# Performance work log

Measured on AMD Instinct MI355X. Metric: run time of the kernel, lower is better.

The kernel has to match this reference:

```python
import jax, jax.numpy as jnp
import numpy as np

B, L, D_MODEL = 2, 1024, 1024
EXPAND = 2
D_INNER = EXPAND * D_MODEL      # 2048
D_STATE = 16
D_CONV = 4
DT_RANK = D_MODEL // 16         # 64


def setup_inputs() -> dict:
    key = jax.random.key(0)
    ks = jax.random.split(key, 8)
    s = 0.02
    x = jax.random.normal(ks[0], (B, L, D_MODEL), jnp.float32)
    W_in = (jax.random.normal(ks[1], (D_MODEL, 2 * D_INNER), jnp.float32) * s)
    conv_w = jax.random.normal(ks[2], (D_INNER, 1, D_CONV), jnp.float32) * 0.2  # depthwise kernel (O,I/g,K)
    conv_b = jnp.zeros((D_INNER,), jnp.float32)
    W_xproj = jax.random.normal(ks[3], (D_INNER, DT_RANK + 2 * D_STATE), jnp.float32) * s
    W_dt = jax.random.normal(ks[4], (DT_RANK, D_INNER), jnp.float32) * (DT_RANK ** -0.5)
    b_dt = jnp.full((D_INNER,), -4.6, jnp.float32)  # softplus^{-1}(~0.01), mamba-style dt init
    A_log = jnp.log(jnp.broadcast_to(jnp.arange(1, D_STATE + 1, dtype=jnp.float32), (D_INNER, D_STATE)))
    D_skip = jnp.ones((D_INNER,), jnp.float32)
    W_out = jax.random.normal(ks[5], (D_INNER, D_MODEL), jnp.float32) * s
    return dict(x=x, W_in=W_in, conv_w=conv_w, conv_b=conv_b, W_xproj=W_xproj,
                W_dt=W_dt, b_dt=b_dt, A_log=A_log, D_skip=D_skip, W_out=W_out)


def _mamba(x, W_in, conv_w, conv_b, W_xproj, W_dt, b_dt, A_log, D_skip, W_out):
    b, l, _ = x.shape
    # input projection and gate split
    xz = jnp.einsum('bld,de->ble', x, W_in)            # (B, L, 2*d_inner)
    x_in, z = jnp.split(xz, 2, axis=-1)                # each (B, L, d_inner)
    # causal depthwise conv1d + SiLU
    xt = jnp.transpose(x_in, (0, 2, 1))                # (B, d_inner, L)
    xt = jnp.pad(xt, ((0, 0), (0, 0), (D_CONV - 1, 0)))
    conv = jax.lax.conv_general_dilated(
        xt, conv_w, window_strides=(1,), padding='VALID',
        dimension_numbers=('NCH', 'OIH', 'NCH'), feature_group_count=D_INNER)
    conv = conv + conv_b[None, :, None]                # (B, d_inner, L)
    u = jax.nn.silu(jnp.transpose(conv, (0, 2, 1)))    # (B, L, d_inner)
    # input-dependent SSM parameters
    x_dbl = jnp.einsum('bld,de->ble', u, W_xproj)      # (B, L, dt_rank + 2*d_state)
    dt_lr = x_dbl[..., :DT_RANK]
    Bm = x_dbl[..., DT_RANK:DT_RANK + D_STATE]         # (B, L, d_state)
    Cm = x_dbl[..., DT_RANK + D_STATE:]                # (B, L, d_state)
    delta = jax.nn.softplus(jnp.einsum('blr,rd->bld', dt_lr, W_dt) + b_dt)  # (B, L, d_inner)
    A = -jnp.exp(A_log)                                # (d_inner, d_state)
    dA = jnp.exp(jnp.einsum('bld,dn->bldn', delta, A))           # (B, L, d_inner, d_state)
    dBu = (delta * u)[..., None] * Bm[:, :, None, :]              # (B, L, d_inner, d_state)
    # selective scan over time
    def step(h, inp):
        dA_t, dBu_t, C_t = inp
        h = dA_t * h + dBu_t                           # (B, d_inner, d_state)
        y_t = jnp.einsum('bdn,bn->bd', h, C_t)
        return h, y_t
    h0 = jnp.zeros((b, D_INNER, D_STATE), x.dtype)
    _, ys = jax.lax.scan(step, h0, (jnp.swapaxes(dA, 0, 1), jnp.swapaxes(dBu, 0, 1), jnp.swapaxes(Cm, 0, 1)))
    y = jnp.swapaxes(ys, 0, 1)                          # (B, L, d_inner)
    y = y + D_skip * u
    y = y * jax.nn.silu(z)
    out = jnp.einsum('bld,de->ble', y, W_out)           # (B, L, d_model)
    return out  # dropout is identity in eval mode


def reference(x, W_in, conv_w, conv_b, W_xproj, W_dt, b_dt, A_log, D_skip, W_out):
    return _mamba(x, W_in, conv_w, conv_b, W_xproj, W_dt, b_dt, A_log, D_skip, W_out)
```

## Files before the change

### kernel.cpp

```cpp
#include <hip/hip_runtime.h>
#include <cmath>

#define B_  2
#define L_  1024
#define DM  1024
#define DI  2048
#define DS  16
#define DR  64
#define NC  32
#define CL  (L_/NC)

typedef __attribute__((ext_vector_type(8))) short short8;
typedef __attribute__((ext_vector_type(4))) float f32x4;

static __device__ __forceinline__ ushort f2bf(float f) {
    union { float f; unsigned u; } c; c.f = f;
    unsigned u = c.u;
    return (ushort)((u + 0x7fffu + ((u >> 16) & 1u)) >> 16);
}
static __device__ __forceinline__ float bf2f(ushort h) {
    union { unsigned u; float f; } c; c.u = ((unsigned)h) << 16;
    return c.f;
}

static __device__ __forceinline__ float softplus_f(float v) {
    return (v > 20.f) ? v : log1pf(__expf(v));
}

static __device__ void bt_body(const float* __restrict__ in,
                               ushort* __restrict__ oh, ushort* __restrict__ ol,
                               int K, int N, int Npad, int bx, int by,
                               float (*t)[33])
{
    const int tid = threadIdx.x;
    const int tx = tid & 31, ty = tid >> 5;
    const int n0 = bx * 32, k0 = by * 32;
    #pragma unroll
    for (int i = 0; i < 4; ++i) {
        int k = k0 + ty * 4 + i, n = n0 + tx;
        t[ty * 4 + i][tx] = (n < N) ? in[(size_t)k * N + n] : 0.f;
    }
    __syncthreads();
    #pragma unroll
    for (int i = 0; i < 4; ++i) {
        int r = n0 + ty * 4 + i;
        int c = k0 + tx;
        if (r < Npad) {
            float v = t[tx][ty * 4 + i];
            ushort h = f2bf(v);
            oh[(size_t)r * K + c] = h;
            if (ol) ol[(size_t)r * K + c] = f2bf(v - bf2f(h));
        }
    }
}

__global__ __launch_bounds__(256) void prep_all(
    const float* __restrict__ x, const float* __restrict__ W_in,
    const float* __restrict__ W_xprj, const float* __restrict__ W_dt,
    ushort* __restrict__ Xh, ushort* __restrict__ WIh, ushort* __restrict__ WIl,
    ushort* __restrict__ WXh, ushort* __restrict__ WXl,
    ushort* __restrict__ WDh, ushort* __restrict__ WDl)
{
    __shared__ float t[32][33];
    int blk = blockIdx.x;
    if (blk < 4096) {
        bt_body(W_in, WIh, WIl, 1024, 4096, 4096, blk & 127, blk >> 7, t);
    } else if (blk < 4352) {
        int b2 = blk - 4096;
        bt_body(W_xprj, WXh, WXl, 2048, 96, 128, b2 & 3, b2 >> 2, t);
    } else if (blk < 4480) {
        int b2 = blk - 4352;
        bt_body(W_dt, WDh, WDl, 64, 2048, 2048, b2 & 63, b2 >> 6, t);
    } else {
        int v = (blk - 4480) * 256 + threadIdx.x;
        int r  = v >> 7;
        int c8 = v & 127;
        const float* p = x + (size_t)r * DM + c8 * 8;
        float4 v0 = *(const float4*)p;
        float4 v1 = *(const float4*)(p + 4);
        float vv[8] = {v0.x, v0.y, v0.z, v0.w, v1.x, v1.y, v1.z, v1.w};
        unsigned h[4];
        #pragma unroll
        for (int j = 0; j < 4; ++j)
            h[j] = (unsigned)f2bf(vv[2*j]) | ((unsigned)f2bf(vv[2*j+1]) << 16);
        size_t o = (size_t)r * 1024 + c8 * 8;
        *(uint4*)&Xh[o] = make_uint4(h[0], h[1], h[2], h[3]);
    }
}

__global__ __launch_bounds__(256) void convBT(
    const float* __restrict__ in, ushort* __restrict__ oh,
    int K, int N, int Npad)
{
    __shared__ float t[32][33];
    bt_body(in, oh, nullptr, K, N, Npad, blockIdx.x, blockIdx.y, t);
}

static __device__ __forceinline__ void stage_tile(
    ushort* lds, const ushort* __restrict__ g, int ld, int row0, int k0,
    int wid, int lane)
{
    #pragma unroll
    for (int it = 0; it < 2; ++it) {
        int o  = wid * 2048 + it * 1024;
        int ob = o + lane * 16;
        int a  = ob ^ (((ob >> 7) & 7) << 4);
        int row = a >> 6;
        int lc  = (a >> 4) & 3;
        const ushort* gp = g + (size_t)(row0 + row) * ld + k0 + lc * 8;
        __builtin_amdgcn_global_load_lds(
            (const __attribute__((address_space(1))) void*)gp,
            (__attribute__((address_space(3))) void*)((char*)lds + o),
            16, 0, 0);
    }
}

template<int TERMS>
static __device__ __forceinline__ void stage_all(
    ushort* buf, const ushort* Ah, const ushort* Bh, const ushort* Bl,
    int lda, int ldb, int bm, int bn, int k, int wid, int lane)
{
    stage_tile(buf,        Ah, lda, bm, k, wid, lane);
    stage_tile(buf + 4096, Bh, ldb, bn, k, wid, lane);
    if (TERMS == 2) stage_tile(buf + 8192, Bl, ldb, bn, k, wid, lane);
}

static __device__ __forceinline__ short8 frag(const ushort* lds, int row, int fq) {
    int a = row * 64 + fq * 16;
    int b = a ^ (((a >> 7) & 7) << 4);
    return *(const short8*)((const char*)lds + b);
}

template<int TERMS>
static __device__ __forceinline__ void compute_tile(
    const ushort* buf, int wr, int wc, int fr, int fq, f32x4 acc[4][4])
{
    const ushort* sAh = buf;
    const ushort* sBh = buf + 4096;
    const ushort* sBl = buf + 8192;
    short8 a_h[4], b_h[4], b_l[4];
    #pragma unroll
    for (int m = 0; m < 4; ++m)
        a_h[m] = frag(sAh, wr + m * 16 + fr, fq);
    #pragma unroll
    for (int n = 0; n < 4; ++n) {
        b_h[n] = frag(sBh, wc + n * 16 + fr, fq);
        if (TERMS == 2) b_l[n] = frag(sBl, wc + n * 16 + fr, fq);
    }
    #pragma unroll
    for (int m = 0; m < 4; ++m)
        #pragma unroll
        for (int n = 0; n < 4; ++n) {
            acc[m][n] = __builtin_amdgcn_mfma_f32_16x16x32_bf16(a_h[m], b_h[n], acc[m][n], 0, 0, 0);
            if (TERMS == 2)
                acc[m][n] = __builtin_amdgcn_mfma_f32_16x16x32_bf16(a_h[m], b_l[n], acc[m][n], 0, 0, 0);
        }
}

template<int TERMS, int EPI>
__global__ __launch_bounds__(256) void gemm_bt(
    const ushort* __restrict__ Ah,
    const ushort* __restrict__ Bh, const ushort* __restrict__ Bl,
    float* __restrict__ C, ushort* __restrict__ oh, ushort* __restrict__ ol,
    const float* __restrict__ bvec,
    int M, int N, int lda, int ldb, int ldc, int kspl)
{
    constexpr int TILE = TERMS == 1 ? 8192 : 12288;
    __shared__ ushort sm[2 * TILE];

    const int tid = threadIdx.x, wid = tid >> 6, lane = tid & 63;
    const int bm = blockIdx.y * 128, bn = blockIdx.x * 128;
    const int kb = blockIdx.z * kspl;
    const int wr = (wid >> 1) * 64, wc = (wid & 1) * 64;
    const int fr = lane & 15, fq = lane >> 4;

    f32x4 acc[4][4] = {};

    stage_all<TERMS>(sm, Ah, Bh, Bl, lda, ldb, bm, bn, kb, wid, lane);
    __syncthreads();
    int cur = 0;
    for (int k0 = 32; k0 < kspl; k0 += 32) {
        ushort* nbuf       = cur ? sm : sm + TILE;
        const ushort* cbuf = cur ? sm + TILE : sm;
        stage_all<TERMS>(nbuf, Ah, Bh, Bl, lda, ldb, bm, bn, kb + k0, wid, lane);
        compute_tile<TERMS>(cbuf, wr, wc, fr, fq, acc);
        __syncthreads();
        cur ^= 1;
    }
    compute_tile<TERMS>(cur ? sm + TILE : sm, wr, wc, fr, fq, acc);

    #pragma unroll
    for (int m = 0; m < 4; ++m) {
        int rbase = bm + wr + m * 16 + fq * 4;
        #pragma unroll
        for (int n = 0; n < 4; ++n) {
            int col = bn + wc + n * 16 + fr;
            if (col >= N) continue;
            if (EPI == 0) {
                #pragma unroll
                for (int j = 0; j < 4; ++j)
                    C[((size_t)blockIdx.z * M + rbase + j) * ldc + col] = acc[m][n][j];
            } else {
                float bb = bvec[col];
                #pragma unroll
                for (int j = 0; j < 4; ++j) {
                    float v = softplus_f(acc[m][n][j] + bb);
                    ushort hh = f2bf(v);
                    size_t off = (size_t)(rbase + j) * ldc + col;
                    oh[off] = hh;
                    ol[off] = f2bf(v - bf2f(hh));
                }
            }
        }
    }
}

__global__ __launch_bounds__(256) void reduce_xproj(
    const float* __restrict__ p, float* __restrict__ xdbl,
    ushort* __restrict__ DTh)
{
    int i = blockIdx.x * 256 + threadIdx.x;
    if (i >= 2048 * 96) return;
    float s = 0.f;
    #pragma unroll
    for (int c = 0; c < 8; ++c) s += p[i + (size_t)c * (2048 * 96)];
    xdbl[i] = s;
    int row = i / 96, col = i - row * 96;
    if (col < 64) DTh[row * 64 + col] = f2bf(s);
}

__global__ __launch_bounds__(256) void reduceN(
    const float* __restrict__ p, float* __restrict__ o, int n, int nch)
{
    int i = blockIdx.x * 256 + threadIdx.x;
    if (i >= n) return;
    float s = 0.f;
    for (int c = 0; c < nch; ++c) s += p[i + (size_t)c * n];
    o[i] = s;
}

__global__ __launch_bounds__(256) void conv_silu(
    const float* __restrict__ xz, const float* __restrict__ w,
    const float* __restrict__ bias, ushort* __restrict__ uh,
    ushort* __restrict__ ul)
{
    int idx = blockIdx.x * 256 + threadIdx.x;
    if (idx >= B_ * L_ * DI) return;
    int d  = idx & (DI - 1);
    int bl = idx >> 11;
    int l  = bl & (L_ - 1);

    const float w0 = w[d * 4 + 0], w1 = w[d * 4 + 1];
    const float w2 = w[d * 4 + 2], w3 = w[d * 4 + 3];
    float s = bias[d];
    size_t base = (size_t)bl * 4096 + d;
    if (l >= 3) s = fmaf(w0, xz[base - 3 * 4096], s);
    if (l >= 2) s = fmaf(w1, xz[base - 2 * 4096], s);
    if (l >= 1) s = fmaf(w2, xz[base - 1 * 4096], s);
    s = fmaf(w3, xz[base], s);
    float v = s / (1.f + __expf(-s));
    ushort h = f2bf(v);
    uh[idx] = h;
    ul[idx] = f2bf(v - bf2f(h));
}

__global__ __launch_bounds__(256) void scan_partial(
    const ushort* __restrict__ Dh, const ushort* __restrict__ Dl,
    const ushort* __restrict__ uh, const ushort* __restrict__ ul,
    const float* __restrict__ xdbl, const float* __restrict__ A_log,
    float* __restrict__ sA, float* __restrict__ sH)
{
    __shared__ float Bs[CL][16];
    const int tid  = threadIdx.x;
    const int dblk = blockIdx.x & 7;
    const int c    = (blockIdx.x >> 3) & (NC - 1);
    const int b    = blockIdx.x >> 8;
    const int d    = dblk * 256 + tid;
    const int bl0  = b * L_ + c * CL;

    for (int i = tid; i < CL * 16; i += 256) {
        int t = i >> 4, n = i & 15;
        Bs[t][n] = xdbl[(size_t)(bl0 + t) * 96 + DR + n];
    }
    __syncthreads();

    float Adn[16];
    #pragma unroll
    for (int q = 0; q < 4; ++q) {
        float4 al = *(const float4*)&A_log[d * DS + q * 4];
        Adn[q * 4 + 0] = -__expf(al.x);
        Adn[q * 4 + 1] = -__expf(al.y);
        Adn[q * 4 + 2] = -__expf(al.z);
        Adn[q * 4 + 3] = -__expf(al.w);
    }
    float h[16];
    #pragma unroll
    for (int n = 0; n < 16; ++n) h[n] = 0.f;
    float S = 0.f;

    size_t pd = (size_t)bl0 * DI + d;
    for (int t = 0; t < CL; ++t) {
        float dv = bf2f(Dh[pd]) + bf2f(Dl[pd]);
        float uv = bf2f(uh[pd]) + bf2f(ul[pd]);
        float du = dv * uv;
        S += dv;
        float Bv[16];
        *(float4*)&Bv[0]  = *(const float4*)&Bs[t][0];
        *(float4*)&Bv[4]  = *(const float4*)&Bs[t][4];
        *(float4*)&Bv[8]  = *(const float4*)&Bs[t][8];
        *(float4*)&Bv[12] = *(const float4*)&Bs[t][12];
        #pragma unroll
        for (int n = 0; n < 16; ++n) {
            float dA = __expf(dv * Adn[n]);
            h[n] = fmaf(dA, h[n], du * Bv[n]);
        }
        pd += DI;
    }

    size_t o = (((size_t)c * B_ + b) * DI + d) * DS;
    float aP[16], hh[16];
    #pragma unroll
    for (int n = 0; n < 16; ++n) { aP[n] = __expf(S * Adn[n]); hh[n] = h[n]; }
    #pragma unroll
    for (int q = 0; q < 4; ++q) {
        *(float4*)&sA[o + q * 4] = *(float4*)&aP[q * 4];
        *(float4*)&sH[o + q * 4] = *(float4*)&hh[q * 4];
    }
}

__global__ __launch_bounds__(256) void scan_combine(
    const float* __restrict__ sA, const float* __restrict__ sH,
    float* __restrict__ hinit)
{
    int idx = blockIdx.x * 256 + threadIdx.x;
    int n = idx & 15;
    int d = (idx >> 4) & (DI - 1);
    int b = idx >> 15;
    float h = 0.f;
    #pragma unroll
    for (int c = 0; c < NC; ++c) {
        size_t o = (((size_t)c * B_ + b) * DI + d) * DS + n;
        hinit[o] = h;
        h = fmaf(sA[o], h, sH[o]);
    }
}

__global__ __launch_bounds__(256) void scan_final(
    const ushort* __restrict__ Dh, const ushort* __restrict__ Dl,
    const ushort* __restrict__ uh, const ushort* __restrict__ ul,
    const float* __restrict__ xdbl, const float* __restrict__ xz,
    const float* __restrict__ A_log, const float* __restrict__ D_skip,
    const float* __restrict__ hinit, ushort* __restrict__ yh)
{
    __shared__ float Bs[CL][16];
    __shared__ float Cs[CL][16];
    const int tid  = threadIdx.x;
    const int dblk = blockIdx.x & 7;
    const int c    = (blockIdx.x >> 3) & (NC - 1);
    const int b    = blockIdx.x >> 8;
    const int d    = dblk * 256 + tid;
    const int bl0  = b * L_ + c * CL;

    for (int i = tid; i < CL * 16; i += 256) {
        int t = i >> 4, n = i & 15;
        size_t px = (size_t)(bl0 + t) * 96 + DR + n;
        Bs[t][n] = xdbl[px];
        Cs[t][n] = xdbl[px + DS];
    }
    __syncthreads();

    float Adn[16];
    #pragma unroll
    for (int q = 0; q < 4; ++q) {
        float4 al = *(const float4*)&A_log[d * DS + q * 4];
        Adn[q * 4 + 0] = -__expf(al.x);
        Adn[q * 4 + 1] = -__expf(al.y);
        Adn[q * 4 + 2] = -__expf(al.z);
        Adn[q * 4 + 3] = -__expf(al.w);
    }
    const float Dd = D_skip[d];

    float h[16];
    size_t o = (((size_t)c * B_ + b) * DI + d) * DS;
    #pragma unroll
    for (int q = 0; q < 4; ++q)
        *(float4*)&h[q * 4] = *(const float4*)&hinit[o + q * 4];

    size_t pd = (size_t)bl0 * DI + d;
    size_t pz = (size_t)bl0 * 4096 + 2048 + d;
    for (int t = 0; t < CL; ++t) {
        float dv = bf2f(Dh[pd]) + bf2f(Dl[pd]);
        float uv = bf2f(uh[pd]) + bf2f(ul[pd]);
        float du = dv * uv;
        float Bv[16], Cv[16];
        *(float4*)&Bv[0]  = *(const float4*)&Bs[t][0];
        *(float4*)&Bv[4]  = *(const float4*)&Bs[t][4];
        *(float4*)&Bv[8]  = *(const float4*)&Bs[t][8];
        *(float4*)&Bv[12] = *(const float4*)&Bs[t][12];
        *(float4*)&Cv[0]  = *(const float4*)&Cs[t][0];
        *(float4*)&Cv[4]  = *(const float4*)&Cs[t][4];
        *(float4*)&Cv[8]  = *(const float4*)&Cs[t][8];
        *(float4*)&Cv[12] = *(const float4*)&Cs[t][12];
        float acc = 0.f;
        #pragma unroll
        for (int n = 0; n < 16; ++n) {
            float dA = __expf(dv * Adn[n]);
            h[n] = fmaf(dA, h[n], du * Bv[n]);
            acc = fmaf(h[n], Cv[n], acc);
        }
        float zv = xz[pz];
        float yv = acc + Dd * uv;
        yv *= zv / (1.f + __expf(-zv));
        yh[pd] = f2bf(yv);
        pd += DI; pz += 4096;
    }
}

extern "C" void kernel_launch(void* const* d_in, const int* in_sizes, int n_in,
                              void* d_out, int out_size, void* d_ws, size_t ws_size,
                              hipStream_t stream)
{
    const float* x      = (const float*)d_in[0];
    const float* W_in   = (const float*)d_in[1];
    const float* conv_w = (const float*)d_in[2];
    const float* conv_b = (const float*)d_in[3];
    const float* W_xprj = (const float*)d_in[4];
    const float* W_dt   = (const float*)d_in[5];
    const float* b_dt   = (const float*)d_in[6];
    const float* A_log  = (const float*)d_in[7];
    const float* D_skip = (const float*)d_in[8];
    const float* W_out  = (const float*)d_in[9];
    float* out = (float*)d_out;

    char* ws = (char*)d_ws;
    float*  xz    = (float*)(ws + 0);
    ushort* Dh    = (ushort*)(ws + 33554432);
    ushort* Dl    = (ushort*)(ws + 41943040);
    float*  xdbl  = (float*)(ws + 50331648);
    ushort* Xh    = (ushort*)(ws + 57409536);
    float*  parts = (float*)(ws + 57409536);
    ushort* WIh   = (ushort*)(ws + 65798144);
    ushort* WIl   = (ushort*)(ws + 74186752);
    float*  sA    = (float*)(ws + 57409536);
    float*  sH    = (float*)(ws + 65798144);
    float*  hin   = (float*)(ws + 74186752);
    ushort* Yh    = (ushort*)(ws + 57409536);
    float*  parts2= (float*)(ws + 65798144);
    ushort* Uh    = (ushort*)(ws + 82575360);
    ushort* Ul    = (ushort*)(ws + 90963968);
    ushort* Woh   = (ushort*)(ws + 82575360);
    ushort* WXh   = (ushort*)(ws + 99352576);
    ushort* WXl   = (ushort*)(ws + 99876864);
    ushort* DTh   = (ushort*)(ws + 100401152);
    ushort* WDh   = (ushort*)(ws + 100914176);
    ushort* WDl   = (ushort*)(ws + 101170688);

    dim3 blk(256);
    const int M = B_ * L_;

    prep_all<<<dim3(5504), blk, 0, stream>>>(
        x, W_in, W_xprj, W_dt, Xh, WIh, WIl, WXh, WXl, WDh, WDl);

    gemm_bt<2, 0><<<dim3(32, 16, 1), blk, 0, stream>>>(
        Xh, WIh, WIl, xz, nullptr, nullptr, nullptr,
        M, 4096, DM, DM, 4096, DM);

    conv_silu<<<dim3((B_ * L_ * DI) / 256), blk, 0, stream>>>(xz, conv_w, conv_b, Uh, Ul);

    gemm_bt<2, 0><<<dim3(1, 16, 8), blk, 0, stream>>>(
        Uh, WXh, WXl, parts, nullptr, nullptr, nullptr,
        M, 96, DI, DI, 96, 256);
    reduce_xproj<<<dim3(768), blk, 0, stream>>>(parts, xdbl, DTh);

    gemm_bt<2, 1><<<dim3(16, 16, 1), blk, 0, stream>>>(
        DTh, WDh, WDl, nullptr, Dh, Dl, b_dt,
        M, DI, DR, DR, DI, DR);

    scan_partial<<<dim3(B_ * NC * 8), blk, 0, stream>>>(
        Dh, Dl, Uh, Ul, xdbl, A_log, sA, sH);
    scan_combine<<<dim3((B_ * DI * DS) / 256), blk, 0, stream>>>(sA, sH, hin);
    scan_final<<<dim3(B_ * NC * 8), blk, 0, stream>>>(
        Dh, Dl, Uh, Ul, xdbl, xz, A_log, D_skip, hin, Yh);

    convBT<<<dim3(DM / 32, DI / 32), blk, 0, stream>>>(W_out, Woh, DI, DM, DM);
    gemm_bt<1, 0><<<dim3(8, 16, 2), blk, 0, stream>>>(
        Yh, Woh, nullptr, parts2, nullptr, nullptr, nullptr,
        M, DM, DI, DI, DM, 1024);
    reduceN<<<dim3(2097152 / 256), blk, 0, stream>>>(parts2, out, M * DM, 2);
}
```

Measured before the change: 204.5 us.

## Drop W_in low-bf16 term and replace split-K out GEMM with 128x64 tile kernel

The input projection GEMM now uses only the high bf16 part of W_in, which removes the hi/lo error-compensation term and the WIl conversion writes. This halves the B-operand staging and MFMA work for the largest GEMM, at the cost of lower precision in xz. The output projection changes from a split-K=2 GEMM followed by a reduction kernel to a dedicated 128x64-tile double-buffered kernel that writes the output directly. That drops the partial buffer traffic and one launch, and raises the block count to 256 so the work still spreads across the GPU.

```diff
diff --git a/kernel.cpp b/kernel.cpp
--- a/kernel.cpp
+++ b/kernel.cpp
@@ -57,14 +57,14 @@
 __global__ __launch_bounds__(256) void prep_all(
     const float* __restrict__ x, const float* __restrict__ W_in,
     const float* __restrict__ W_xprj, const float* __restrict__ W_dt,
-    ushort* __restrict__ Xh, ushort* __restrict__ WIh, ushort* __restrict__ WIl,
+    ushort* __restrict__ Xh, ushort* __restrict__ WIh,
     ushort* __restrict__ WXh, ushort* __restrict__ WXl,
     ushort* __restrict__ WDh, ushort* __restrict__ WDl)
 {
     __shared__ float t[32][33];
     int blk = blockIdx.x;
     if (blk < 4096) {
-        bt_body(W_in, WIh, WIl, 1024, 4096, 4096, blk & 127, blk >> 7, t);
+        bt_body(W_in, WIh, nullptr, 1024, 4096, 4096, blk & 127, blk >> 7, t);
     } else if (blk < 4352) {
         int b2 = blk - 4096;
         bt_body(W_xprj, WXh, WXl, 2048, 96, 128, b2 & 3, b2 >> 2, t);
@@ -115,6 +115,28 @@
     }
 }
 
+static __device__ __forceinline__ void stage_tile64(
+    ushort* lds, const ushort* __restrict__ g, int ld, int row0, int k0,
+    int wid, int lane)
+{
+    int o  = wid * 1024;
+    int ob = o + lane * 16;
+    int a  = ob ^ (((ob >> 7) & 7) << 4);
+    int row = a >> 6;
+    int lc  = (a >> 4) & 3;
+    const ushort* gp = g + (size_t)(row0 + row) * ld + k0 + lc * 8;
+    __builtin_amdgcn_global_load_lds(
+        (const __attribute__((address_space(1))) void*)gp,
+        (__attribute__((address_space(3))) void*)((char*)lds + o),
+        16, 0, 0);
+}
+
+static __device__ __forceinline__ short8 frag(const ushort* lds, int row, int fq) {
+    int a = row * 64 + fq * 16;
+    int b = a ^ (((a >> 7) & 7) << 4);
+    return *(const short8*)((const char*)lds + b);
+}
+
 template<int TERMS>
 static __device__ __forceinline__ void stage_all(
     ushort* buf, const ushort* Ah, const ushort* Bh, const ushort* Bl,
@@ -123,12 +145,6 @@
     stage_tile(buf,        Ah, lda, bm, k, wid, lane);
     stage_tile(buf + 4096, Bh, ldb, bn, k, wid, lane);
     if (TERMS == 2) stage_tile(buf + 8192, Bl, ldb, bn, k, wid, lane);
-}
-
-static __device__ __forceinline__ short8 frag(const ushort* lds, int row, int fq) {
-    int a = row * 64 + fq * 16;
-    int b = a ^ (((a >> 7) & 7) << 4);
-    return *(const short8*)((const char*)lds + b);
 }
 
 template<int TERMS>
@@ -215,6 +231,73 @@
     }
 }
 
+__global__ __launch_bounds__(256) void gemm_out64(
+    const ushort* __restrict__ Ah, const ushort* __restrict__ Bh,
+    float* __restrict__ C, int K, int lda, int ldb, int ldc)
+{
+    __shared__ ushort sm[12288];
+    const int tid = threadIdx.x, wid = tid >> 6, lane = tid & 63;
+    const int bm = blockIdx.y * 128, bn = blockIdx.x * 64;
+    const int wr = (wid >> 1) * 64, wc = (wid & 1) * 32;
+    const int fr = lane & 15, fq = lane >> 4;
+
+    f32x4 acc[4][2] = {};
+
+    stage_tile  (sm,        Ah, lda, bm, 0, wid, lane);
+    stage_tile64(sm + 4096, Bh, ldb, bn, 0, wid, lane);
+    __syncthreads();
+    int cur = 0;
+    for (int k0 = 32; k0 < K; k0 += 32) {
+        ushort* nbuf       = cur ? sm : sm + 6144;
+        const ushort* cbuf = cur ? sm + 6144 : sm;
+        stage_tile  (nbuf,        Ah, lda, bm, k0, wid, lane);
+        stage_tile64(nbuf + 4096, Bh, ldb, bn, k0, wid, lane);
+        {
+            short8 a_h[4], b_h[2];
+            #pragma unroll
+            for (int m = 0; m < 4; ++m)
+                a_h[m] = frag(cbuf, wr + m * 16 + fr, fq);
+            #pragma unroll
+            for (int n = 0; n < 2; ++n)
+                b_h[n] = frag(cbuf + 4096, wc + n * 16 + fr, fq);
+            #pragma unroll
+            for (int m = 0; m < 4; ++m)
+                #pragma unroll
+                for (int n = 0; n < 2; ++n)
+                    acc[m][n] = __builtin_amdgcn_mfma_f32_16x16x32_bf16(a_h[m], b_h[n], acc[m][n], 0, 0, 0);
+        }
+        __syncthreads();
+        cur ^= 1;
+    }
+    {
+        const ushort* cbuf = cur ? sm + 6144 : sm;
+        short8 a_h[4], b_h[2];
+        #pragma unroll
+        for (int m = 0; m < 4; ++m)
+            a_h[m] = frag(cbuf, wr + m * 16 + fr, fq);
+        #pragma unroll
+        for (int n = 0; n < 2; ++n)
+            b_h[n] = frag(cbuf + 4096, wc + n * 16 + fr, fq);
+        #pragma unroll
+        for (int m = 0; m < 4; ++m)
+            #pragma unroll
+            for (int n = 0; n < 2; ++n)
+                acc[m][n] = __builtin_amdgcn_mfma_f32_16x16x32_bf16(a_h[m], b_h[n], acc[m][n], 0, 0, 0);
+    }
+
+    #pragma unroll
+    for (int m = 0; m < 4; ++m) {
+        int rbase = bm + wr + m * 16 + fq * 4;
+        #pragma unroll
+        for (int n = 0; n < 2; ++n) {
+            int col = bn + wc + n * 16 + fr;
+            #pragma unroll
+            for (int j = 0; j < 4; ++j)
+                C[(size_t)(rbase + j) * ldc + col] = acc[m][n][j];
+        }
+    }
+}
+
 __global__ __launch_bounds__(256) void reduce_xproj(
     const float* __restrict__ p, float* __restrict__ xdbl,
     ushort* __restrict__ DTh)
@@ -227,16 +310,6 @@
     xdbl[i] = s;
     int row = i / 96, col = i - row * 96;
     if (col < 64) DTh[row * 64 + col] = f2bf(s);
-}
-
-__global__ __launch_bounds__(256) void reduceN(
-    const float* __restrict__ p, float* __restrict__ o, int n, int nch)
-{
-    int i = blockIdx.x * 256 + threadIdx.x;
-    if (i >= n) return;
-    float s = 0.f;
-    for (int c = 0; c < nch; ++c) s += p[i + (size_t)c * n];
-    o[i] = s;
 }
 
 __global__ __launch_bounds__(256) void conv_silu(
@@ -440,12 +513,10 @@
     ushort* Xh    = (ushort*)(ws + 57409536);
     float*  parts = (float*)(ws + 57409536);
     ushort* WIh   = (ushort*)(ws + 65798144);
-    ushort* WIl   = (ushort*)(ws + 74186752);
     float*  sA    = (float*)(ws + 57409536);
     float*  sH    = (float*)(ws + 65798144);
     float*  hin   = (float*)(ws + 74186752);
     ushort* Yh    = (ushort*)(ws + 57409536);
-    float*  parts2= (float*)(ws + 65798144);
     ushort* Uh    = (ushort*)(ws + 82575360);
     ushort* Ul    = (ushort*)(ws + 90963968);
     ushort* Woh   = (ushort*)(ws + 82575360);
@@ -459,10 +530,10 @@
     const int M = B_ * L_;
 
     prep_all<<<dim3(5504), blk, 0, stream>>>(
-        x, W_in, W_xprj, W_dt, Xh, WIh, WIl, WXh, WXl, WDh, WDl);
-
-    gemm_bt<2, 0><<<dim3(32, 16, 1), blk, 0, stream>>>(
-        Xh, WIh, WIl, xz, nullptr, nullptr, nullptr,
+        x, W_in, W_xprj, W_dt, Xh, WIh, WXh, WXl, WDh, WDl);
+
+    gemm_bt<1, 0><<<dim3(32, 16, 1), blk, 0, stream>>>(
+        Xh, WIh, nullptr, xz, nullptr, nullptr, nullptr,
         M, 4096, DM, DM, 4096, DM);
 
     conv_silu<<<dim3((B_ * L_ * DI) / 256), blk, 0, stream>>>(xz, conv_w, conv_b, Uh, Ul);
@@ -483,8 +554,6 @@
         Dh, Dl, Uh, Ul, xdbl, xz, A_log, D_skip, hin, Yh);
 
     convBT<<<dim3(DM / 32, DI / 32), blk, 0, stream>>>(W_out, Woh, DI, DM, DM);
-    gemm_bt<1, 0><<<dim3(8, 16, 2), blk, 0, stream>>>(
-        Yh, Woh, nullptr, parts2, nullptr, nullptr, nullptr,
-        M, DM, DI, DI, DM, 1024);
-    reduceN<<<dim3(2097152 / 256), blk, 0, stream>>>(parts2, out, M * DM, 2);
-}
+    gemm_out64<<<dim3(DM / 64, M / 128), blk, 0, stream>>>(
+        Yh, Woh, out, DI, DI, DI, DM);
+}
```

After: 181.9 us. 1.12x faster.
